# Kernel optimization log

Measured on AMD Instinct MI355X. Metric: run time of the kernel, lower is better.

## Reference

```python
import jax, jax.numpy as jnp
import numpy as np

B, N_LEAVES, HID, NCLS, VOCAB = 32, 512, 128, 2, 50257
N_NODES = 2 * N_LEAVES - 1  # complete binary tree, heap layout


def setup_inputs() -> dict:
    key = jax.random.key(0)
    ks = jax.random.split(key, 12)
    x = jax.random.randint(ks[0], (B, N_NODES), 0, VOCAB)
    cue = jax.random.randint(ks[1], (B, N_NODES), 0, NCLS)
    # word j sits at tree leaf node L-1+j
    word_index = jnp.tile(jnp.arange(N_LEAVES - 1, 2 * N_LEAVES - 1), (B, 1))
    # parent->child adjacency stored in adj[:, 1]
    A = np.zeros((2, N_NODES, N_NODES), dtype=bool)
    p = np.arange(N_LEAVES - 1)
    A[1, p, 2 * p + 1] = True
    A[1, p, 2 * p + 2] = True
    adj = jnp.asarray(np.broadcast_to(A, (B, 2, N_NODES, N_NODES)).copy())
    s = 0.05
    emb = jax.random.normal(ks[2], (VOCAB, HID - NCLS)) * s
    Wc = jax.random.normal(ks[3], (HID, 2 * HID)) * s
    bc = jax.random.normal(ks[4], (HID,)) * s
    Wd = jax.random.normal(ks[5], (2 * HID, 2 * HID)) * s
    bd = jax.random.normal(ks[6], (2 * HID,)) * s
    Wg = jax.random.normal(ks[7], (HID, HID)) * s
    bg = jax.random.normal(ks[8], (HID,)) * s
    Wcl = jax.random.normal(ks[9], (NCLS, 2 * HID)) * s
    bcl = jax.random.normal(ks[10], (NCLS,)) * s
    return dict(x=x, word_index=word_index, cue=cue, adj=adj, emb=emb,
                Wc=Wc, bc=bc, Wd=Wd, bd=bd, Wg=Wg, bg=bg, Wcl=Wcl, bcl=bcl)


def reference(x, word_index, cue, adj, emb, Wc, bc, Wd, bd, Wg, bg, Wcl, bcl):
    # adj encodes the same complete binary heap tree that is hardcoded below
    Bn, N = x.shape
    H = Wc.shape[0]
    C = bcl.shape[0]
    L = (N + 1) // 2
    depth = L.bit_length() - 1  # leaves live at level `depth`
    bidx = jnp.arange(Bn)[:, None]

    word_emb = emb[x]                                   # (B, N, H-C)
    cue_oh = jax.nn.one_hot(cue, C, dtype=word_emb.dtype)
    in_feats = jnp.concatenate([word_emb, cue_oh], -1)  # (B, N, H)
    sent = in_feats[bidx, word_index]                   # (B, L, H) leaf feats

    # ---- upward compose: level-batched bottom-up traversal ----
    h = jnp.zeros((Bn, N, H), in_feats.dtype).at[bidx, word_index].set(sent)
    for d in range(depth - 1, -1, -1):
        p = jnp.arange(2 ** d - 1, 2 ** (d + 1) - 1)
        ctx = jnp.concatenate([h[:, 2 * p + 1], h[:, 2 * p + 2]], -1)  # (B, 2^d, 2H)
        h = h.at[:, p].set(jnp.tanh(ctx @ Wc.T + bc))
    # upward_results never writes leaf rows -> leaves stay zero
    up = h.at[bidx, word_index].set(0.0)

    g_down = jax.nn.sigmoid(h[:, 0] @ Wg.T + bg)        # (B, H)

    # ---- downward decompose: level-batched top-down traversal ----
    down = jnp.zeros_like(h).at[:, 0].set(g_down)
    for d in range(depth):
        p = jnp.arange(2 ** d - 1, 2 ** (d + 1) - 1)
        ctx = jnp.concatenate([down[:, p], up[:, p]], -1)
        ch = jnp.tanh(ctx @ Wd.T + bd)                  # (B, 2^d, 2H)
        down = down.at[:, 2 * p + 1].set(ch[..., :H]).at[:, 2 * p + 2].set(ch[..., H:])

    tree = jnp.concatenate([down, up], -1)              # (B, N, 2H)
    scores = jax.nn.sigmoid(tree @ Wcl.T + bcl)
    return jax.nn.softmax(scores, -1)
```

## Files before the change

### kernel.cpp

```cpp
#include <hip/hip_runtime.h>
#include <hip/hip_fp16.h>


constexpr int NNODES = 1023;

typedef _Float16 h2 __attribute__((ext_vector_type(2)));

__device__ __forceinline__ float dot2(uint a, uint b, float c) {
  union { uint u; h2 h; } x, y;
  x.u = a; y.u = b;
  return __builtin_amdgcn_fdot2(x.h, y.h, c, false);
}

__device__ __forceinline__ uint f2h2(float a, float b) {
  return (uint)__half_as_ushort(__float2half_rn(a)) |
         ((uint)__half_as_ushort(__float2half_rn(b)) << 16);
}

__device__ __forceinline__ float2 h2f2(uint u) {
  union { uint u; h2 h; } c; c.u = u;
  return make_float2((float)c.h.x, (float)c.h.y);
}

__device__ __forceinline__ void load_wslice(const float* __restrict__ Wrow,
                                            int l16, int m, uint* wout) {
  const float4 f0 = *(const float4*)(Wrow + l16 * 8 + m * 128);
  const float4 f1 = *(const float4*)(Wrow + l16 * 8 + m * 128 + 4);
  wout[0] = f2h2(f0.x, f0.y);
  wout[1] = f2h2(f0.z, f0.w);
  wout[2] = f2h2(f1.x, f1.y);
  wout[3] = f2h2(f1.z, f1.w);
}

__device__ __forceinline__ float fold16(const float* a, int l) {
  float b[8];
#pragma unroll
  for (int u = 0; u < 8; ++u) {
    const float mine = (l & 1) ? a[2 * u + 1] : a[2 * u];
    const float oth  = (l & 1) ? a[2 * u]     : a[2 * u + 1];
    b[u] = mine + __shfl_xor(oth, 1);
  }
  float c[4];
#pragma unroll
  for (int u = 0; u < 4; ++u) {
    const float mine = (l & 2) ? b[2 * u + 1] : b[2 * u];
    const float oth  = (l & 2) ? b[2 * u]     : b[2 * u + 1];
    c[u] = mine + __shfl_xor(oth, 2);
  }
  float d[2];
#pragma unroll
  for (int u = 0; u < 2; ++u) {
    const float mine = (l & 4) ? c[2 * u + 1] : c[2 * u];
    const float oth  = (l & 4) ? c[2 * u]     : c[2 * u + 1];
    d[u] = mine + __shfl_xor(oth, 4);
  }
  const float mine = (l & 8) ? d[1] : d[0];
  const float oth  = (l & 8) ? d[0] : d[1];
  return mine + __shfl_xor(oth, 8);
}

__device__ __forceinline__ float fold8(const float* a, int l) {
  float b[4];
#pragma unroll
  for (int u = 0; u < 4; ++u) {
    const float mine = (l & 1) ? a[2 * u + 1] : a[2 * u];
    const float oth  = (l & 1) ? a[2 * u]     : a[2 * u + 1];
    b[u] = mine + __shfl_xor(oth, 1);
  }
  float c[2];
#pragma unroll
  for (int u = 0; u < 2; ++u) {
    const float mine = (l & 2) ? b[2 * u + 1] : b[2 * u];
    const float oth  = (l & 2) ? b[2 * u]     : b[2 * u + 1];
    c[u] = mine + __shfl_xor(oth, 2);
  }
  const float mine = (l & 4) ? c[1] : c[0];
  const float oth  = (l & 4) ? c[0] : c[1];
  return mine + __shfl_xor(oth, 4);
}

__device__ __forceinline__ float fold4(const float* a, int l) {
  float b[2];
#pragma unroll
  for (int u = 0; u < 2; ++u) {
    const float mine = (l & 1) ? a[2 * u + 1] : a[2 * u];
    const float oth  = (l & 1) ? a[2 * u]     : a[2 * u + 1];
    b[u] = mine + __shfl_xor(oth, 1);
  }
  const float mine = (l & 2) ? b[1] : b[0];
  const float oth  = (l & 2) ? b[0] : b[1];
  return mine + __shfl_xor(oth, 2);
}

template<int CH>
__device__ __forceinline__ float foldCH(const float (&a)[CH * 4], int l16) {
  if constexpr (CH == 4) {
    return fold16(a, l16);
  } else if constexpr (CH == 2) {
    float t = fold8(a, l16);
    t += __shfl_xor(t, 8);
    return t;
  } else {
    float t = fold4(a, l16);
    t += __shfl_xor(t, 4);
    t += __shfl_xor(t, 8);
    return t;
  }
}

template<int CH>
__device__ __forceinline__ void up_pass(uint* __restrict__ heap2, int base, int cb,
                                        int cbase, const uint (&w)[4][8],
                                        float bias_r, int g, int l16, bool wr) {
  float a[CH * 4];
#pragma unroll
  for (int v = 0; v < CH * 4; ++v) a[v] = 0.f;
#pragma unroll
  for (int p = 0; p < CH; ++p) {
    const uint* cp = heap2 + (cb + 2 * (cbase + p)) * 64 + l16 * 4;
#pragma unroll
    for (int m = 0; m < 2; ++m) {
      const uint4 cc = *(const uint4*)(cp + m * 64);
#pragma unroll
      for (int r = 0; r < 4; ++r) {
        float av = a[p * 4 + r];
        av = dot2(w[r][m * 4 + 0], cc.x, av);
        av = dot2(w[r][m * 4 + 1], cc.y, av);
        av = dot2(w[r][m * 4 + 2], cc.z, av);
        av = dot2(w[r][m * 4 + 3], cc.w, av);
        a[p * 4 + r] = av;
      }
    }
  }
  const float tot = foldCH<CH>(a, l16);
  if (wr && l16 < CH * 4) {
    _Float16* hH = (_Float16*)heap2;
    hH[(base + cbase + (l16 >> 2)) * 128 + 4 * g + (l16 & 3)] =
        (_Float16)tanhf(tot + bias_r);
  }
}

template<int NP, int NH>
__device__ __forceinline__ void up_level16(uint* __restrict__ heap2,
                                           const uint (&w)[4][8],
                                           float bias_r, int g, int l16, int ph) {
  constexpr int base = NP - 1, cb = 2 * NP - 1;
  if constexpr (NP >= 4 * NH) {
#pragma unroll
    for (int c0 = 0; c0 < NP; c0 += 4 * NH)
      up_pass<4>(heap2, base, cb, c0 + ph * 4, w, bias_r, g, l16, true);
  } else if constexpr (NP * 2 == 4 * NH) {
    up_pass<2>(heap2, base, cb, ph * 2, w, bias_r, g, l16, true);
  } else if constexpr (NP == NH) {
    up_pass<1>(heap2, base, cb, ph, w, bias_r, g, l16, true);
  } else {
    up_pass<1>(heap2, base, cb, 0, w, bias_r, g, l16, ph == 0);
  }
  __syncthreads();
}

template<int CH>
__device__ __forceinline__ void down_pass(uint* __restrict__ db2,
                                          const uint* __restrict__ ub2,
                                          int base, int cb, int cbase,
                                          const uint (&w)[4][8],
                                          float bias_r, int g, int l16) {
  float a[CH * 4];
#pragma unroll
  for (int v = 0; v < CH * 4; ++v) a[v] = 0.f;
#pragma unroll
  for (int p = 0; p < CH; ++p) {
    const uint* dp = db2 + (base + cbase + p) * 64 + l16 * 4;
    const uint* up = ub2 + (base + cbase + p) * 64 + l16 * 4;
    const uint4 c0 = *(const uint4*)dp;
    const uint4 c1 = *(const uint4*)up;
#pragma unroll
    for (int r = 0; r < 4; ++r) {
      float av = a[p * 4 + r];
      av = dot2(w[r][0], c0.x, av);
      av = dot2(w[r][1], c0.y, av);
      av = dot2(w[r][2], c0.z, av);
      av = dot2(w[r][3], c0.w, av);
      av = dot2(w[r][4], c1.x, av);
      av = dot2(w[r][5], c1.y, av);
      av = dot2(w[r][6], c1.z, av);
      av = dot2(w[r][7], c1.w, av);
      a[p * 4 + r] = av;
    }
  }
  const float tot = foldCH<CH>(a, l16);
  if (l16 < CH * 4) {
    const int row = 4 * g + (l16 & 3);
    ((_Float16*)db2)[(cb + 2 * (cbase + (l16 >> 2)) + (row >> 7)) * 128 + (row & 127)] =
        (_Float16)tanhf(tot + bias_r);
  }
}

template<int NP>
__device__ __forceinline__ void down_level16(uint* __restrict__ db2,
                                             const uint* __restrict__ ub2,
                                             const uint (&w)[4][8],
                                             float bias_r, int g, int l16) {
  constexpr int base = NP - 1, cb = 2 * NP - 1;
  if constexpr (NP >= 4) {
#pragma unroll
    for (int c0 = 0; c0 < NP; c0 += 4)
      down_pass<4>(db2, ub2, base, cb, c0, w, bias_r, g, l16);
  } else {
    down_pass<NP>(db2, ub2, base, cb, 0, w, bias_r, g, l16);
  }
  __syncthreads();
}

template<int NP>
__device__ __forceinline__ void down_level16_dual(uint* __restrict__ A0,
                                                  const uint* __restrict__ B0,
                                                  uint* __restrict__ A1,
                                                  const uint* __restrict__ B1,
                                                  const uint (&w)[4][8],
                                                  float bias_r, int g, int l16) {
  constexpr int base = NP - 1, cb = 2 * NP - 1;
  if constexpr (NP >= 4) {
#pragma unroll
    for (int c0 = 0; c0 < NP; c0 += 4) {
      down_pass<4>(A0, B0, base, cb, c0, w, bias_r, g, l16);
      down_pass<4>(A1, B1, base, cb, c0, w, bias_r, g, l16);
    }
  } else {
    down_pass<NP>(A0, B0, base, cb, 0, w, bias_r, g, l16);
    down_pass<NP>(A1, B1, base, cb, 0, w, bias_r, g, l16);
  }
  __syncthreads();
}

__device__ __forceinline__ void classify16(const uint* __restrict__ dn2,
                                           const uint* __restrict__ un2,
                                           const float* __restrict__ wcl,
                                           const float* __restrict__ bcl,
                                           float* __restrict__ o, int l16) {
  const int k0 = l16 * 8;
  float s0 = 0.f, s1 = 0.f;
  {
    const uint4 du = *(const uint4*)(dn2 + l16 * 4);
    const float2 d0 = h2f2(du.x), d1 = h2f2(du.y), d2 = h2f2(du.z), d3 = h2f2(du.w);
    s0 += d0.x * wcl[k0]     + d0.y * wcl[k0 + 1] + d1.x * wcl[k0 + 2] + d1.y * wcl[k0 + 3]
        + d2.x * wcl[k0 + 4] + d2.y * wcl[k0 + 5] + d3.x * wcl[k0 + 6] + d3.y * wcl[k0 + 7];
    s1 += d0.x * wcl[256 + k0]     + d0.y * wcl[256 + k0 + 1]
        + d1.x * wcl[256 + k0 + 2] + d1.y * wcl[256 + k0 + 3]
        + d2.x * wcl[256 + k0 + 4] + d2.y * wcl[256 + k0 + 5]
        + d3.x * wcl[256 + k0 + 6] + d3.y * wcl[256 + k0 + 7];
  }
  if (un2) {
    const uint4 uu = *(const uint4*)(un2 + l16 * 4);
    const float2 u0 = h2f2(uu.x), u1 = h2f2(uu.y), u2 = h2f2(uu.z), u3 = h2f2(uu.w);
    s0 += u0.x * wcl[128 + k0]     + u0.y * wcl[128 + k0 + 1]
        + u1.x * wcl[128 + k0 + 2] + u1.y * wcl[128 + k0 + 3]
        + u2.x * wcl[128 + k0 + 4] + u2.y * wcl[128 + k0 + 5]
        + u3.x * wcl[128 + k0 + 6] + u3.y * wcl[128 + k0 + 7];
    s1 += u0.x * wcl[384 + k0]     + u0.y * wcl[384 + k0 + 1]
        + u1.x * wcl[384 + k0 + 2] + u1.y * wcl[384 + k0 + 3]
        + u2.x * wcl[384 + k0 + 4] + u2.y * wcl[384 + k0 + 5]
        + u3.x * wcl[384 + k0 + 6] + u3.y * wcl[384 + k0 + 7];
  }
#pragma unroll
  for (int m = 8; m >= 1; m >>= 1) {
    s0 += __shfl_xor(s0, m);
    s1 += __shfl_xor(s1, m);
  }
  if (l16 == 0) {
    s0 += bcl[0]; s1 += bcl[1];
    const float p0 = 1.f / (1.f + expf(-s0));
    const float p1 = 1.f / (1.f + expf(-s1));
    const float mx = fmaxf(p0, p1);
    const float e0 = expf(p0 - mx), e1 = expf(p1 - mx);
    const float inv = 1.f / (e0 + e1);
    o[0] = e0 * inv;
    o[1] = e1 * inv;
  }
}

__global__ __launch_bounds__(512, 4) void kA_up(const int* __restrict__ x,
                                                const int* __restrict__ cue,
                                                const float* __restrict__ emb,
                                                const float* __restrict__ Wc,
                                                const float* __restrict__ bc,
                                                uint* __restrict__ hw) {
  __shared__ __align__(16) uint heap2[63 * 64];
  __shared__ __align__(16) uint pad[10240];
  const int b = blockIdx.x >> 4, s = blockIdx.x & 15, r = 15 + s;
  const int t = threadIdx.x, g = t >> 4, l16 = t & 15;
  if (t == 0) ((volatile uint*)pad)[0] = 0u;

  uint w[4][8];
#pragma unroll
  for (int rr = 0; rr < 4; ++rr)
#pragma unroll
    for (int m = 0; m < 2; ++m)
      load_wslice(Wc + (4 * g + rr) * 256, l16, m, &w[rr][m * 4]);
  const float bias_r = bc[4 * g + (l16 & 3)];

  for (int idx = t; idx < 32 * 64; idx += 512) {
    const int j = idx >> 6, c = idx & 63, k0 = 2 * c;
    const int gq = ((r + 1) << 5) - 1 + j;
    const int xi = x[b * NNODES + gq], ci = cue[b * NNODES + gq];
    const float v0 = (k0 < 126) ? emb[(long long)xi * 126 + k0]
                                : ((ci == (k0 - 126)) ? 1.f : 0.f);
    const float v1 = (k0 + 1 < 126) ? emb[(long long)xi * 126 + k0 + 1]
                                    : ((ci == (k0 + 1 - 126)) ? 1.f : 0.f);
    heap2[(31 + j) * 64 + c] = f2h2(v0, v1);
  }
  __syncthreads();

  up_level16<16, 1>(heap2, w, bias_r, g, l16, 0);
  up_level16<8, 1>(heap2, w, bias_r, g, l16, 0);
  up_level16<4, 1>(heap2, w, bias_r, g, l16, 0);
  up_level16<2, 1>(heap2, w, bias_r, g, l16, 0);
  up_level16<1, 1>(heap2, w, bias_r, g, l16, 0);

  uint4* dst = (uint4*)(hw + (size_t)(b * 16 + s) * 31 * 64);
  const uint4* src = (const uint4*)heap2;
  for (int idx = t; idx < 31 * 16; idx += 512) dst[idx] = src[idx];
}

__global__ __launch_bounds__(1024, 4) void kC_all(const float* __restrict__ Wc,
                                                  const float* __restrict__ bc,
                                                  const float* __restrict__ Wg,
                                                  const float* __restrict__ bg,
                                                  const float* __restrict__ Wd,
                                                  const float* __restrict__ bd,
                                                  const float* __restrict__ Wcl,
                                                  const float* __restrict__ bcl,
                                                  const uint* __restrict__ hw,
                                                  float* __restrict__ out) {
  __shared__ __align__(16) uint A2[2 * 63 * 64];
  __shared__ __align__(16) uint B2[2 * 31 * 64];
  __shared__ __align__(16) uint rootdn2[128];
  __shared__ __align__(16) float wcl[512];
  __shared__ __align__(16) uint pad[8192];
  const int b = blockIdx.x >> 3, sp = blockIdx.x & 7;
  const int t = threadIdx.x, g = t >> 4, l16 = t & 15;
  if (t == 0) ((volatile uint*)pad)[0] = 0u;
  uint* A1 = A2 + 63 * 64;
  uint* B1 = B2 + 31 * 64;

  for (int idx = t; idx < 16 * 16; idx += 1024) {
    const int s = idx >> 4, q = idx & 15;
    *((uint4*)(B2 + (15 + s) * 64) + q) =
        *((const uint4*)(hw + (size_t)(b * 16 + s) * 31 * 64) + q);
  }
  if (t < 512) wcl[t] = Wcl[t];
  __syncthreads();

  {
    const int gu = g & 31, ph = t >> 9;
    uint wu[4][8];
#pragma unroll
    for (int rr = 0; rr < 4; ++rr)
#pragma unroll
      for (int m = 0; m < 2; ++m)
        load_wslice(Wc + (4 * gu + rr) * 256, l16, m, &wu[rr][m * 4]);
    const float bias_u = bc[4 * gu + (l16 & 3)];
    up_level16<8, 2>(B2, wu, bias_u, gu, l16, ph);
    up_level16<4, 2>(B2, wu, bias_u, gu, l16, ph);
    up_level16<2, 2>(B2, wu, bias_u, gu, l16, ph);
    up_level16<1, 2>(B2, wu, bias_u, gu, l16, ph);

    uint wg[4][4];
#pragma unroll
    for (int rr = 0; rr < 4; ++rr)
      load_wslice(Wg + (4 * gu + rr) * 128, l16, 0, &wg[rr][0]);
    float a[4];
#pragma unroll
    for (int v = 0; v < 4; ++v) a[v] = 0.f;
    {
      const uint4 cc = *(const uint4*)(B2 + l16 * 4);
#pragma unroll
      for (int rr = 0; rr < 4; ++rr) {
        float av = a[rr];
        av = dot2(wg[rr][0], cc.x, av);
        av = dot2(wg[rr][1], cc.y, av);
        av = dot2(wg[rr][2], cc.z, av);
        av = dot2(wg[rr][3], cc.w, av);
        a[rr] = av;
      }
    }
    float tot = fold4(a, l16);
    tot += __shfl_xor(tot, 4);
    tot += __shfl_xor(tot, 8);
    if (ph == 0 && l16 < 4) {
      const int row = 4 * gu + l16;
      ((_Float16*)A2)[row] = (_Float16)(1.f / (1.f + expf(-(tot + bg[row]))));
    }
    __syncthreads();
  }
  asm volatile("" ::: "memory");

  uint w[4][8];
#pragma unroll
  for (int rr = 0; rr < 4; ++rr)
#pragma unroll
    for (int m = 0; m < 2; ++m)
      load_wslice(Wd + (4 * g + rr) * 256, l16, m, &w[rr][m * 4]);
  const float bias_r = bd[4 * g + (l16 & 3)];

  down_level16<1>(A2, B2, w, bias_r, g, l16);
  down_level16<2>(A2, B2, w, bias_r, g, l16);
  down_level16<4>(A2, B2, w, bias_r, g, l16);
  down_level16<8>(A2, B2, w, bias_r, g, l16);

  if (sp == 0 && t < 15 * 16) {
    const int m = t >> 4;
    classify16(A2 + m * 64, B2 + m * 64, wcl, bcl,
               out + ((size_t)b * NNODES + m) * 2, l16);
  }
  if (t < 128) rootdn2[t] = A2[(15 + sp * 2 + (t >> 6)) * 64 + (t & 63)];
  __syncthreads();

  for (int idx = t; idx < 2 * 31 * 16; idx += 1024) {
    const int ss = (idx >= 31 * 16) ? 1 : 0;
    const int k4 = idx - ss * 31 * 16;
    ((uint4*)(B2 + ss * 31 * 64))[k4] =
        ((const uint4*)(hw + (size_t)(b * 16 + sp * 2 + ss) * 31 * 64))[k4];
  }
  if (t < 128) A2[(t >> 6) * 63 * 64 + (t & 63)] = rootdn2[t];
  __syncthreads();

  down_level16_dual<1>(A2, B2, A1, B1, w, bias_r, g, l16);
  down_level16_dual<2>(A2, B2, A1, B1, w, bias_r, g, l16);
  down_level16_dual<4>(A2, B2, A1, B1, w, bias_r, g, l16);
  down_level16_dual<8>(A2, B2, A1, B1, w, bias_r, g, l16);
  down_level16_dual<16>(A2, B2, A1, B1, w, bias_r, g, l16);

  if (t < 63 * 16) {
    const int m = t >> 4;
    const int lvl = 31 - __clz(m + 1);
    const int j = (m + 1) - (1 << lvl);
#pragma unroll
    for (int ss = 0; ss < 2; ++ss) {
      const int r = 15 + sp * 2 + ss;
      const int gq = ((r + 1) << lvl) - 1 + j;
      classify16(A2 + ss * 63 * 64 + m * 64,
                 (m < 31) ? (B2 + ss * 31 * 64 + m * 64) : nullptr, wcl, bcl,
                 out + ((size_t)b * NNODES + gq) * 2, l16);
    }
  }
}

extern "C" void kernel_launch(void* const* d_in, const int* in_sizes, int n_in,
                              void* d_out, int out_size, void* d_ws, size_t ws_size,
                              hipStream_t stream) {
  const int*   x   = (const int*)d_in[0];
  const int*   cue = (const int*)d_in[2];
  const float* emb = (const float*)d_in[4];
  const float* Wc  = (const float*)d_in[5];
  const float* bc  = (const float*)d_in[6];
  const float* Wd  = (const float*)d_in[7];
  const float* bd  = (const float*)d_in[8];
  const float* Wg  = (const float*)d_in[9];
  const float* bg  = (const float*)d_in[10];
  const float* Wcl = (const float*)d_in[11];
  const float* bcl = (const float*)d_in[12];
  float* out = (float*)d_out;

  uint* hw = (uint*)d_ws;

  hipLaunchKernelGGL(kA_up,  dim3(512), dim3(512), 0, stream, x, cue, emb, Wc, bc, hw);
  hipLaunchKernelGGL(kC_all, dim3(256), dim3(1024), 0, stream,
                     Wc, bc, Wg, bg, Wd, bd, Wcl, bcl, hw, out);
}
```

Measured before the change: 70.38 us.

## Split downward pass into one 512-thread block per subtree with paired row weights

The second kernel now runs 512 blocks of 512 threads, each owning a single 32-leaf subtree, where before it ran 256 blocks of 1024 threads that each handled two subtrees. Each thread keeps weights for both output halves (rows r and r+128) and computes both child outputs in one pass, which doubles the per-thread weight registers. The top-of-tree upward/downward work (levels above the subtrees) is now recomputed redundantly by 16 blocks per batch instead of 8. This trades more redundant top-level work and register pressure for more, smaller blocks and higher occupancy.

```diff
diff --git a/kernel.cpp b/kernel.cpp
--- a/kernel.cpp
+++ b/kernel.cpp
@@ -111,7 +111,7 @@
 template<int CH>
 __device__ __forceinline__ void up_pass(uint* __restrict__ heap2, int base, int cb,
                                         int cbase, const uint (&w)[4][8],
-                                        float bias_r, int g, int l16, bool wr) {
+                                        float bias_r, int g, int l16) {
   float a[CH * 4];
 #pragma unroll
   for (int v = 0; v < CH * 4; ++v) a[v] = 0.f;
@@ -133,102 +133,88 @@
     }
   }
   const float tot = foldCH<CH>(a, l16);
-  if (wr && l16 < CH * 4) {
-    _Float16* hH = (_Float16*)heap2;
-    hH[(base + cbase + (l16 >> 2)) * 128 + 4 * g + (l16 & 3)] =
+  if (l16 < CH * 4) {
+    ((_Float16*)heap2)[(base + cbase + (l16 >> 2)) * 128 + 4 * g + (l16 & 3)] =
         (_Float16)tanhf(tot + bias_r);
   }
 }
 
-template<int NP, int NH>
-__device__ __forceinline__ void up_level16(uint* __restrict__ heap2,
-                                           const uint (&w)[4][8],
-                                           float bias_r, int g, int l16, int ph) {
-  constexpr int base = NP - 1, cb = 2 * NP - 1;
-  if constexpr (NP >= 4 * NH) {
-#pragma unroll
-    for (int c0 = 0; c0 < NP; c0 += 4 * NH)
-      up_pass<4>(heap2, base, cb, c0 + ph * 4, w, bias_r, g, l16, true);
-  } else if constexpr (NP * 2 == 4 * NH) {
-    up_pass<2>(heap2, base, cb, ph * 2, w, bias_r, g, l16, true);
-  } else if constexpr (NP == NH) {
-    up_pass<1>(heap2, base, cb, ph, w, bias_r, g, l16, true);
-  } else {
-    up_pass<1>(heap2, base, cb, 0, w, bias_r, g, l16, ph == 0);
-  }
-  __syncthreads();
-}
-
-template<int CH>
-__device__ __forceinline__ void down_pass(uint* __restrict__ db2,
-                                          const uint* __restrict__ ub2,
-                                          int base, int cb, int cbase,
-                                          const uint (&w)[4][8],
-                                          float bias_r, int g, int l16) {
-  float a[CH * 4];
-#pragma unroll
-  for (int v = 0; v < CH * 4; ++v) a[v] = 0.f;
-#pragma unroll
-  for (int p = 0; p < CH; ++p) {
-    const uint* dp = db2 + (base + cbase + p) * 64 + l16 * 4;
-    const uint* up = ub2 + (base + cbase + p) * 64 + l16 * 4;
-    const uint4 c0 = *(const uint4*)dp;
-    const uint4 c1 = *(const uint4*)up;
-#pragma unroll
-    for (int r = 0; r < 4; ++r) {
-      float av = a[p * 4 + r];
-      av = dot2(w[r][0], c0.x, av);
-      av = dot2(w[r][1], c0.y, av);
-      av = dot2(w[r][2], c0.z, av);
-      av = dot2(w[r][3], c0.w, av);
-      av = dot2(w[r][4], c1.x, av);
-      av = dot2(w[r][5], c1.y, av);
-      av = dot2(w[r][6], c1.z, av);
-      av = dot2(w[r][7], c1.w, av);
-      a[p * 4 + r] = av;
-    }
-  }
-  const float tot = foldCH<CH>(a, l16);
-  if (l16 < CH * 4) {
-    const int row = 4 * g + (l16 & 3);
-    ((_Float16*)db2)[(cb + 2 * (cbase + (l16 >> 2)) + (row >> 7)) * 128 + (row & 127)] =
-        (_Float16)tanhf(tot + bias_r);
-  }
-}
-
 template<int NP>
-__device__ __forceinline__ void down_level16(uint* __restrict__ db2,
-                                             const uint* __restrict__ ub2,
-                                             const uint (&w)[4][8],
-                                             float bias_r, int g, int l16) {
+__device__ __forceinline__ void up_level512(uint* __restrict__ heap2,
+                                            const uint (&w)[4][8],
+                                            float bias_r, int g, int l16) {
   constexpr int base = NP - 1, cb = 2 * NP - 1;
   if constexpr (NP >= 4) {
 #pragma unroll
     for (int c0 = 0; c0 < NP; c0 += 4)
-      down_pass<4>(db2, ub2, base, cb, c0, w, bias_r, g, l16);
+      up_pass<4>(heap2, base, cb, c0, w, bias_r, g, l16);
   } else {
-    down_pass<NP>(db2, ub2, base, cb, 0, w, bias_r, g, l16);
-  }
-  __syncthreads();
+    up_pass<NP>(heap2, base, cb, 0, w, bias_r, g, l16);
+  }
+  __syncthreads();
+}
+
+template<int CH>
+__device__ __forceinline__ void down_pass8(uint* __restrict__ db2,
+                                           const uint* __restrict__ ub2,
+                                           int base, int cb, int cbase,
+                                           const uint (&w)[2][4][8],
+                                           float bias0, float bias1,
+                                           int g, int l16) {
+  float a0[CH * 4], a1[CH * 4];
+#pragma unroll
+  for (int v = 0; v < CH * 4; ++v) { a0[v] = 0.f; a1[v] = 0.f; }
+#pragma unroll
+  for (int p = 0; p < CH; ++p) {
+    const uint4 c0 = *(const uint4*)(db2 + (base + cbase + p) * 64 + l16 * 4);
+    const uint4 c1 = *(const uint4*)(ub2 + (base + cbase + p) * 64 + l16 * 4);
+#pragma unroll
+    for (int r = 0; r < 4; ++r) {
+      float av = a0[p * 4 + r];
+      av = dot2(w[0][r][0], c0.x, av);
+      av = dot2(w[0][r][1], c0.y, av);
+      av = dot2(w[0][r][2], c0.z, av);
+      av = dot2(w[0][r][3], c0.w, av);
+      av = dot2(w[0][r][4], c1.x, av);
+      av = dot2(w[0][r][5], c1.y, av);
+      av = dot2(w[0][r][6], c1.z, av);
+      av = dot2(w[0][r][7], c1.w, av);
+      a0[p * 4 + r] = av;
+      float bv = a1[p * 4 + r];
+      bv = dot2(w[1][r][0], c0.x, bv);
+      bv = dot2(w[1][r][1], c0.y, bv);
+      bv = dot2(w[1][r][2], c0.z, bv);
+      bv = dot2(w[1][r][3], c0.w, bv);
+      bv = dot2(w[1][r][4], c1.x, bv);
+      bv = dot2(w[1][r][5], c1.y, bv);
+      bv = dot2(w[1][r][6], c1.z, bv);
+      bv = dot2(w[1][r][7], c1.w, bv);
+      a1[p * 4 + r] = bv;
+    }
+  }
+  const float t0 = foldCH<CH>(a0, l16);
+  const float t1 = foldCH<CH>(a1, l16);
+  if (l16 < CH * 4) {
+    const int p = l16 >> 2, col = 4 * g + (l16 & 3);
+    _Float16* dH = (_Float16*)db2;
+    dH[(cb + 2 * (cbase + p)) * 128 + col]     = (_Float16)tanhf(t0 + bias0);
+    dH[(cb + 2 * (cbase + p) + 1) * 128 + col] = (_Float16)tanhf(t1 + bias1);
+  }
 }
 
 template<int NP>
-__device__ __forceinline__ void down_level16_dual(uint* __restrict__ A0,
-                                                  const uint* __restrict__ B0,
-                                                  uint* __restrict__ A1,
-                                                  const uint* __restrict__ B1,
-                                                  const uint (&w)[4][8],
-                                                  float bias_r, int g, int l16) {
+__device__ __forceinline__ void down_level8(uint* __restrict__ db2,
+                                            const uint* __restrict__ ub2,
+                                            const uint (&w)[2][4][8],
+                                            float bias0, float bias1,
+                                            int g, int l16) {
   constexpr int base = NP - 1, cb = 2 * NP - 1;
   if constexpr (NP >= 4) {
 #pragma unroll
-    for (int c0 = 0; c0 < NP; c0 += 4) {
-      down_pass<4>(A0, B0, base, cb, c0, w, bias_r, g, l16);
-      down_pass<4>(A1, B1, base, cb, c0, w, bias_r, g, l16);
-    }
+    for (int c0 = 0; c0 < NP; c0 += 4)
+      down_pass8<4>(db2, ub2, base, cb, c0, w, bias0, bias1, g, l16);
   } else {
-    down_pass<NP>(A0, B0, base, cb, 0, w, bias_r, g, l16);
-    down_pass<NP>(A1, B1, base, cb, 0, w, bias_r, g, l16);
+    down_pass8<NP>(db2, ub2, base, cb, 0, w, bias0, bias1, g, l16);
   }
   __syncthreads();
 }
@@ -311,18 +297,18 @@
   }
   __syncthreads();
 
-  up_level16<16, 1>(heap2, w, bias_r, g, l16, 0);
-  up_level16<8, 1>(heap2, w, bias_r, g, l16, 0);
-  up_level16<4, 1>(heap2, w, bias_r, g, l16, 0);
-  up_level16<2, 1>(heap2, w, bias_r, g, l16, 0);
-  up_level16<1, 1>(heap2, w, bias_r, g, l16, 0);
+  up_level512<16>(heap2, w, bias_r, g, l16);
+  up_level512<8>(heap2, w, bias_r, g, l16);
+  up_level512<4>(heap2, w, bias_r, g, l16);
+  up_level512<2>(heap2, w, bias_r, g, l16);
+  up_level512<1>(heap2, w, bias_r, g, l16);
 
   uint4* dst = (uint4*)(hw + (size_t)(b * 16 + s) * 31 * 64);
   const uint4* src = (const uint4*)heap2;
   for (int idx = t; idx < 31 * 16; idx += 512) dst[idx] = src[idx];
 }
 
-__global__ __launch_bounds__(1024, 4) void kC_all(const float* __restrict__ Wc,
+__global__ __launch_bounds__(512, 4) void kS_down(const float* __restrict__ Wc,
                                                   const float* __restrict__ bc,
                                                   const float* __restrict__ Wg,
                                                   const float* __restrict__ bg,
@@ -332,43 +318,40 @@
                                                   const float* __restrict__ bcl,
                                                   const uint* __restrict__ hw,
                                                   float* __restrict__ out) {
-  __shared__ __align__(16) uint A2[2 * 63 * 64];
-  __shared__ __align__(16) uint B2[2 * 31 * 64];
-  __shared__ __align__(16) uint rootdn2[128];
+  __shared__ __align__(16) uint A2[63 * 64];
+  __shared__ __align__(16) uint B2[31 * 64];
+  __shared__ __align__(16) uint rootdn2[64];
   __shared__ __align__(16) float wcl[512];
-  __shared__ __align__(16) uint pad[8192];
-  const int b = blockIdx.x >> 3, sp = blockIdx.x & 7;
+  __shared__ __align__(16) uint pad[8500];
+  const int b = blockIdx.x >> 4, s = blockIdx.x & 15;
   const int t = threadIdx.x, g = t >> 4, l16 = t & 15;
   if (t == 0) ((volatile uint*)pad)[0] = 0u;
-  uint* A1 = A2 + 63 * 64;
-  uint* B1 = B2 + 31 * 64;
-
-  for (int idx = t; idx < 16 * 16; idx += 1024) {
-    const int s = idx >> 4, q = idx & 15;
-    *((uint4*)(B2 + (15 + s) * 64) + q) =
-        *((const uint4*)(hw + (size_t)(b * 16 + s) * 31 * 64) + q);
+
+  for (int idx = t; idx < 16 * 16; idx += 512) {
+    const int s2 = idx >> 4, q = idx & 15;
+    *((uint4*)(B2 + (15 + s2) * 64) + q) =
+        *((const uint4*)(hw + (size_t)(b * 16 + s2) * 31 * 64) + q);
   }
   if (t < 512) wcl[t] = Wcl[t];
   __syncthreads();
 
   {
-    const int gu = g & 31, ph = t >> 9;
     uint wu[4][8];
 #pragma unroll
     for (int rr = 0; rr < 4; ++rr)
 #pragma unroll
       for (int m = 0; m < 2; ++m)
-        load_wslice(Wc + (4 * gu + rr) * 256, l16, m, &wu[rr][m * 4]);
-    const float bias_u = bc[4 * gu + (l16 & 3)];
-    up_level16<8, 2>(B2, wu, bias_u, gu, l16, ph);
-    up_level16<4, 2>(B2, wu, bias_u, gu, l16, ph);
-    up_level16<2, 2>(B2, wu, bias_u, gu, l16, ph);
-    up_level16<1, 2>(B2, wu, bias_u, gu, l16, ph);
+        load_wslice(Wc + (4 * g + rr) * 256, l16, m, &wu[rr][m * 4]);
+    const float bias_u = bc[4 * g + (l16 & 3)];
+    up_level512<8>(B2, wu, bias_u, g, l16);
+    up_level512<4>(B2, wu, bias_u, g, l16);
+    up_level512<2>(B2, wu, bias_u, g, l16);
+    up_level512<1>(B2, wu, bias_u, g, l16);
 
     uint wg[4][4];
 #pragma unroll
     for (int rr = 0; rr < 4; ++rr)
-      load_wslice(Wg + (4 * gu + rr) * 128, l16, 0, &wg[rr][0]);
+      load_wslice(Wg + (4 * g + rr) * 128, l16, 0, &wg[rr][0]);
     float a[4];
 #pragma unroll
     for (int v = 0; v < 4; ++v) a[v] = 0.f;
@@ -387,60 +370,58 @@
     float tot = fold4(a, l16);
     tot += __shfl_xor(tot, 4);
     tot += __shfl_xor(tot, 8);
-    if (ph == 0 && l16 < 4) {
-      const int row = 4 * gu + l16;
+    if (l16 < 4) {
+      const int row = 4 * g + l16;
       ((_Float16*)A2)[row] = (_Float16)(1.f / (1.f + expf(-(tot + bg[row]))));
     }
     __syncthreads();
   }
   asm volatile("" ::: "memory");
 
-  uint w[4][8];
-#pragma unroll
-  for (int rr = 0; rr < 4; ++rr)
-#pragma unroll
-    for (int m = 0; m < 2; ++m)
-      load_wslice(Wd + (4 * g + rr) * 256, l16, m, &w[rr][m * 4]);
-  const float bias_r = bd[4 * g + (l16 & 3)];
-
-  down_level16<1>(A2, B2, w, bias_r, g, l16);
-  down_level16<2>(A2, B2, w, bias_r, g, l16);
-  down_level16<4>(A2, B2, w, bias_r, g, l16);
-  down_level16<8>(A2, B2, w, bias_r, g, l16);
-
-  if (sp == 0 && t < 15 * 16) {
+  uint w[2][4][8];
+#pragma unroll
+  for (int h = 0; h < 2; ++h)
+#pragma unroll
+    for (int rr = 0; rr < 4; ++rr)
+#pragma unroll
+      for (int m = 0; m < 2; ++m)
+        load_wslice(Wd + (h * 128 + 4 * g + rr) * 256, l16, m, &w[h][rr][m * 4]);
+  const float bias0 = bd[4 * g + (l16 & 3)];
+  const float bias1 = bd[128 + 4 * g + (l16 & 3)];
+
+  down_level8<1>(A2, B2, w, bias0, bias1, g, l16);
+  down_level8<2>(A2, B2, w, bias0, bias1, g, l16);
+  down_level8<4>(A2, B2, w, bias0, bias1, g, l16);
+  down_level8<8>(A2, B2, w, bias0, bias1, g, l16);
+
+  if (s == 0 && t < 15 * 16) {
     const int m = t >> 4;
     classify16(A2 + m * 64, B2 + m * 64, wcl, bcl,
                out + ((size_t)b * NNODES + m) * 2, l16);
   }
-  if (t < 128) rootdn2[t] = A2[(15 + sp * 2 + (t >> 6)) * 64 + (t & 63)];
-  __syncthreads();
-
-  for (int idx = t; idx < 2 * 31 * 16; idx += 1024) {
-    const int ss = (idx >= 31 * 16) ? 1 : 0;
-    const int k4 = idx - ss * 31 * 16;
-    ((uint4*)(B2 + ss * 31 * 64))[k4] =
-        ((const uint4*)(hw + (size_t)(b * 16 + sp * 2 + ss) * 31 * 64))[k4];
-  }
-  if (t < 128) A2[(t >> 6) * 63 * 64 + (t & 63)] = rootdn2[t];
-  __syncthreads();
-
-  down_level16_dual<1>(A2, B2, A1, B1, w, bias_r, g, l16);
-  down_level16_dual<2>(A2, B2, A1, B1, w, bias_r, g, l16);
-  down_level16_dual<4>(A2, B2, A1, B1, w, bias_r, g, l16);
-  down_level16_dual<8>(A2, B2, A1, B1, w, bias_r, g, l16);
-  down_level16_dual<16>(A2, B2, A1, B1, w, bias_r, g, l16);
-
-  if (t < 63 * 16) {
-    const int m = t >> 4;
-    const int lvl = 31 - __clz(m + 1);
-    const int j = (m + 1) - (1 << lvl);
-#pragma unroll
-    for (int ss = 0; ss < 2; ++ss) {
-      const int r = 15 + sp * 2 + ss;
+  if (t < 64) rootdn2[t] = A2[(15 + s) * 64 + t];
+  __syncthreads();
+
+  for (int idx = t; idx < 31 * 16; idx += 512)
+    ((uint4*)B2)[idx] = ((const uint4*)(hw + (size_t)(b * 16 + s) * 31 * 64))[idx];
+  if (t < 64) A2[t] = rootdn2[t];
+  __syncthreads();
+
+  down_level8<1>(A2, B2, w, bias0, bias1, g, l16);
+  down_level8<2>(A2, B2, w, bias0, bias1, g, l16);
+  down_level8<4>(A2, B2, w, bias0, bias1, g, l16);
+  down_level8<8>(A2, B2, w, bias0, bias1, g, l16);
+  down_level8<16>(A2, B2, w, bias0, bias1, g, l16);
+
+  const int r = 15 + s;
+#pragma unroll
+  for (int pass = 0; pass < 2; ++pass) {
+    const int m = (t >> 4) + pass * 32;
+    if (m < 63) {
+      const int lvl = 31 - __clz(m + 1);
+      const int j = (m + 1) - (1 << lvl);
       const int gq = ((r + 1) << lvl) - 1 + j;
-      classify16(A2 + ss * 63 * 64 + m * 64,
-                 (m < 31) ? (B2 + ss * 31 * 64 + m * 64) : nullptr, wcl, bcl,
+      classify16(A2 + m * 64, (m < 31) ? (B2 + m * 64) : nullptr, wcl, bcl,
                  out + ((size_t)b * NNODES + gq) * 2, l16);
     }
   }
@@ -464,7 +445,7 @@
 
   uint* hw = (uint*)d_ws;
 
-  hipLaunchKernelGGL(kA_up,  dim3(512), dim3(512), 0, stream, x, cue, emb, Wc, bc, hw);
-  hipLaunchKernelGGL(kC_all, dim3(256), dim3(1024), 0, stream,
+  hipLaunchKernelGGL(kA_up,   dim3(512), dim3(512), 0, stream, x, cue, emb, Wc, bc, hw);
+  hipLaunchKernelGGL(kS_down, dim3(512), dim3(512), 0, stream,
                      Wc, bc, Wg, bg, Wd, bd, Wcl, bcl, hw, out);
 }
```

Result: slower. 76.40 us (+8.6%).

## Fuse up and down passes into one cooperative kernel with grid syncs

Applied to the files above, without the earlier changes.

Replaces the two-kernel pipeline with a single cooperative kernel. Each 1024-thread block handles two subtrees, then exchanges subtree roots through global memory with grid-wide syncs instead of a second launch. Block 0 of each batch builds the top of the tree and the root-down state, and the leaf-level down pass now computes both child halves per thread group. This removes a launch and the round trip of full subtree heaps, at the cost of two grid barriers, idle blocks during the top-tree phase, and higher register use. The old two-kernel path is kept as a fallback if the cooperative launch fails.

```diff
diff --git a/kernel.cpp b/kernel.cpp
--- a/kernel.cpp
+++ b/kernel.cpp
@@ -1,5 +1,8 @@
 #include <hip/hip_runtime.h>
 #include <hip/hip_fp16.h>
+#include <hip/hip_cooperative_groups.h>
+
+namespace cg = cooperative_groups;
 
 
 constexpr int NNODES = 1023;
@@ -20,6 +23,13 @@
 __device__ __forceinline__ float2 h2f2(uint u) {
   union { uint u; h2 h; } c; c.u = u;
   return make_float2((float)c.h.x, (float)c.h.y);
+}
+
+__device__ __forceinline__ void gstore(uint* p, uint v) {
+  __hip_atomic_store(p, v, __ATOMIC_RELEASE, __HIP_MEMORY_SCOPE_AGENT);
+}
+__device__ __forceinline__ uint gload(const uint* p) {
+  return __hip_atomic_load(p, __ATOMIC_ACQUIRE, __HIP_MEMORY_SCOPE_AGENT);
 }
 
 __device__ __forceinline__ void load_wslice(const float* __restrict__ Wrow,
@@ -134,24 +144,38 @@
   }
   const float tot = foldCH<CH>(a, l16);
   if (wr && l16 < CH * 4) {
-    _Float16* hH = (_Float16*)heap2;
-    hH[(base + cbase + (l16 >> 2)) * 128 + 4 * g + (l16 & 3)] =
+    ((_Float16*)heap2)[(base + cbase + (l16 >> 2)) * 128 + 4 * g + (l16 & 3)] =
         (_Float16)tanhf(tot + bias_r);
   }
 }
 
-template<int NP, int NH>
-__device__ __forceinline__ void up_level16(uint* __restrict__ heap2,
-                                           const uint (&w)[4][8],
-                                           float bias_r, int g, int l16, int ph) {
+template<int NP>
+__device__ __forceinline__ void up_level512(uint* __restrict__ heap2,
+                                            const uint (&w)[4][8],
+                                            float bias_r, int g, int l16) {
   constexpr int base = NP - 1, cb = 2 * NP - 1;
-  if constexpr (NP >= 4 * NH) {
-#pragma unroll
-    for (int c0 = 0; c0 < NP; c0 += 4 * NH)
+  if constexpr (NP >= 4) {
+#pragma unroll
+    for (int c0 = 0; c0 < NP; c0 += 4)
+      up_pass<4>(heap2, base, cb, c0, w, bias_r, g, l16, true);
+  } else {
+    up_pass<NP>(heap2, base, cb, 0, w, bias_r, g, l16, true);
+  }
+  __syncthreads();
+}
+
+template<int NP>
+__device__ __forceinline__ void up_level16x2(uint* __restrict__ heap2,
+                                             const uint (&w)[4][8],
+                                             float bias_r, int g, int l16, int ph) {
+  constexpr int base = NP - 1, cb = 2 * NP - 1;
+  if constexpr (NP >= 8) {
+#pragma unroll
+    for (int c0 = 0; c0 < NP; c0 += 8)
       up_pass<4>(heap2, base, cb, c0 + ph * 4, w, bias_r, g, l16, true);
-  } else if constexpr (NP * 2 == 4 * NH) {
+  } else if constexpr (NP == 4) {
     up_pass<2>(heap2, base, cb, ph * 2, w, bias_r, g, l16, true);
-  } else if constexpr (NP == NH) {
+  } else if constexpr (NP == 2) {
     up_pass<1>(heap2, base, cb, ph, w, bias_r, g, l16, true);
   } else {
     up_pass<1>(heap2, base, cb, 0, w, bias_r, g, l16, ph == 0);
@@ -170,10 +194,8 @@
   for (int v = 0; v < CH * 4; ++v) a[v] = 0.f;
 #pragma unroll
   for (int p = 0; p < CH; ++p) {
-    const uint* dp = db2 + (base + cbase + p) * 64 + l16 * 4;
-    const uint* up = ub2 + (base + cbase + p) * 64 + l16 * 4;
-    const uint4 c0 = *(const uint4*)dp;
-    const uint4 c1 = *(const uint4*)up;
+    const uint4 c0 = *(const uint4*)(db2 + (base + cbase + p) * 64 + l16 * 4);
+    const uint4 c1 = *(const uint4*)(ub2 + (base + cbase + p) * 64 + l16 * 4);
 #pragma unroll
     for (int r = 0; r < 4; ++r) {
       float av = a[p * 4 + r];
@@ -229,6 +251,73 @@
   } else {
     down_pass<NP>(A0, B0, base, cb, 0, w, bias_r, g, l16);
     down_pass<NP>(A1, B1, base, cb, 0, w, bias_r, g, l16);
+  }
+  __syncthreads();
+}
+
+template<int CH>
+__device__ __forceinline__ void down_pass8(uint* __restrict__ db2,
+                                           const uint* __restrict__ ub2,
+                                           uint* __restrict__ wr,
+                                           int base, int cb, int cbase,
+                                           const uint (&w)[2][4][8],
+                                           float bias0, float bias1,
+                                           int g, int l16) {
+  float a0[CH * 4], a1[CH * 4];
+#pragma unroll
+  for (int v = 0; v < CH * 4; ++v) { a0[v] = 0.f; a1[v] = 0.f; }
+#pragma unroll
+  for (int p = 0; p < CH; ++p) {
+    const uint4 c0 = *(const uint4*)(db2 + (base + cbase + p) * 64 + l16 * 4);
+    const uint4 c1 = *(const uint4*)(ub2 + (base + cbase + p) * 64 + l16 * 4);
+#pragma unroll
+    for (int r = 0; r < 4; ++r) {
+      float av = a0[p * 4 + r];
+      av = dot2(w[0][r][0], c0.x, av);
+      av = dot2(w[0][r][1], c0.y, av);
+      av = dot2(w[0][r][2], c0.z, av);
+      av = dot2(w[0][r][3], c0.w, av);
+      av = dot2(w[0][r][4], c1.x, av);
+      av = dot2(w[0][r][5], c1.y, av);
+      av = dot2(w[0][r][6], c1.z, av);
+      av = dot2(w[0][r][7], c1.w, av);
+      a0[p * 4 + r] = av;
+      float bv = a1[p * 4 + r];
+      bv = dot2(w[1][r][0], c0.x, bv);
+      bv = dot2(w[1][r][1], c0.y, bv);
+      bv = dot2(w[1][r][2], c0.z, bv);
+      bv = dot2(w[1][r][3], c0.w, bv);
+      bv = dot2(w[1][r][4], c1.x, bv);
+      bv = dot2(w[1][r][5], c1.y, bv);
+      bv = dot2(w[1][r][6], c1.z, bv);
+      bv = dot2(w[1][r][7], c1.w, bv);
+      a1[p * 4 + r] = bv;
+    }
+  }
+  const float t0 = foldCH<CH>(a0, l16);
+  const float t1 = foldCH<CH>(a1, l16);
+  if (l16 < CH * 4) {
+    const int p = l16 >> 2, col = 4 * g + (l16 & 3);
+    _Float16* dH = (_Float16*)wr;
+    dH[(cb + 2 * (cbase + p)) * 128 + col]     = (_Float16)tanhf(t0 + bias0);
+    dH[(cb + 2 * (cbase + p) + 1) * 128 + col] = (_Float16)tanhf(t1 + bias1);
+  }
+}
+
+template<int NP>
+__device__ __forceinline__ void down_level8(uint* __restrict__ db2,
+                                            const uint* __restrict__ ub2,
+                                            uint* __restrict__ wr,
+                                            const uint (&w)[2][4][8],
+                                            float bias0, float bias1,
+                                            int g, int l16) {
+  constexpr int base = NP - 1, cb = 2 * NP - 1;
+  if constexpr (NP >= 4) {
+#pragma unroll
+    for (int c0 = 0; c0 < NP; c0 += 4)
+      down_pass8<4>(db2, ub2, wr, base, cb, c0, w, bias0, bias1, g, l16);
+  } else {
+    down_pass8<NP>(db2, ub2, wr, base, cb, 0, w, bias0, bias1, g, l16);
   }
   __syncthreads();
 }
@@ -279,7 +368,178 @@
   }
 }
 
-__global__ __launch_bounds__(512, 4) void kA_up(const int* __restrict__ x,
+__device__ __forceinline__ void gather_leaves(uint* __restrict__ heapX,
+                                              const int* __restrict__ x,
+                                              const int* __restrict__ cue,
+                                              const float* __restrict__ emb,
+                                              int b, int r, int tt, int stride) {
+  for (int idx = tt; idx < 32 * 64; idx += stride) {
+    const int j = idx >> 6, c = idx & 63, k0 = 2 * c;
+    const int gq = ((r + 1) << 5) - 1 + j;
+    const int xi = x[b * NNODES + gq], ci = cue[b * NNODES + gq];
+    const float v0 = (k0 < 126) ? emb[(long long)xi * 126 + k0]
+                                : ((ci == (k0 - 126)) ? 1.f : 0.f);
+    const float v1 = (k0 + 1 < 126) ? emb[(long long)xi * 126 + k0 + 1]
+                                    : ((ci == (k0 + 1 - 126)) ? 1.f : 0.f);
+    heapX[(31 + j) * 64 + c] = f2h2(v0, v1);
+  }
+}
+
+__global__ __launch_bounds__(1024, 4) void kFused(const int* __restrict__ x,
+                                                  const int* __restrict__ cue,
+                                                  const float* __restrict__ emb,
+                                                  const float* __restrict__ Wc,
+                                                  const float* __restrict__ bc,
+                                                  const float* __restrict__ Wg,
+                                                  const float* __restrict__ bg,
+                                                  const float* __restrict__ Wd,
+                                                  const float* __restrict__ bd,
+                                                  const float* __restrict__ Wcl,
+                                                  const float* __restrict__ bcl,
+                                                  uint* __restrict__ roots,
+                                                  uint* __restrict__ rootdn,
+                                                  float* __restrict__ out) {
+  __shared__ __align__(16) uint heapA[63 * 64];
+  __shared__ __align__(16) uint heapB[63 * 64];
+  __shared__ __align__(16) uint dbA[31 * 64];
+  __shared__ __align__(16) uint dbB[31 * 64];
+  __shared__ __align__(16) float wcl[512];
+  __shared__ __align__(16) uint pad[8448];
+  const int b = blockIdx.x >> 3, sp = blockIdx.x & 7;
+  const int t = threadIdx.x;
+  const int h = t >> 9, tt = t & 511, g = tt >> 4, l16 = t & 15;
+  const int s = sp * 2 + h, r = 15 + s;
+  uint* heapX = h ? heapB : heapA;
+  uint* dbX   = h ? dbB : dbA;
+  if (t == 0) ((volatile uint*)pad)[0] = 0u;
+  cg::grid_group grid = cg::this_grid();
+
+  uint wu[4][8];
+#pragma unroll
+  for (int rr = 0; rr < 4; ++rr)
+#pragma unroll
+    for (int m = 0; m < 2; ++m)
+      load_wslice(Wc + (4 * g + rr) * 256, l16, m, &wu[rr][m * 4]);
+  const float bias_u = bc[4 * g + (l16 & 3)];
+  if (t < 512) wcl[t] = Wcl[t];
+
+  gather_leaves(heapX, x, cue, emb, b, r, tt, 512);
+  __syncthreads();
+
+  up_level512<16>(heapX, wu, bias_u, g, l16);
+  up_level512<8>(heapX, wu, bias_u, g, l16);
+  up_level512<4>(heapX, wu, bias_u, g, l16);
+  up_level512<2>(heapX, wu, bias_u, g, l16);
+  up_level512<1>(heapX, wu, bias_u, g, l16);
+
+  if (tt < 64) gstore(&roots[(size_t)(b * 16 + s) * 64 + tt], heapX[tt]);
+  grid.sync();
+
+  if (sp == 0) {
+    uint* mub = dbA;
+    uint* mdb = dbB;
+    for (int idx = t; idx < 16 * 64; idx += 1024) {
+      const int s2 = idx >> 6, c = idx & 63;
+      mub[(15 + s2) * 64 + c] = gload(&roots[(size_t)(b * 16 + s2) * 64 + c]);
+    }
+    __syncthreads();
+
+    up_level16x2<8>(mub, wu, bias_u, g, l16, h);
+    up_level16x2<4>(mub, wu, bias_u, g, l16, h);
+    up_level16x2<2>(mub, wu, bias_u, g, l16, h);
+    up_level16x2<1>(mub, wu, bias_u, g, l16, h);
+
+    {
+      uint wg[4][4];
+#pragma unroll
+      for (int rr = 0; rr < 4; ++rr)
+        load_wslice(Wg + (4 * g + rr) * 128, l16, 0, &wg[rr][0]);
+      float a[4];
+#pragma unroll
+      for (int v = 0; v < 4; ++v) a[v] = 0.f;
+      const uint4 cc = *(const uint4*)(mub + l16 * 4);
+#pragma unroll
+      for (int rr = 0; rr < 4; ++rr) {
+        float av = a[rr];
+        av = dot2(wg[rr][0], cc.x, av);
+        av = dot2(wg[rr][1], cc.y, av);
+        av = dot2(wg[rr][2], cc.z, av);
+        av = dot2(wg[rr][3], cc.w, av);
+        a[rr] = av;
+      }
+      float tot = fold4(a, l16);
+      tot += __shfl_xor(tot, 4);
+      tot += __shfl_xor(tot, 8);
+      if (h == 0 && l16 < 4) {
+        const int row = 4 * g + l16;
+        ((_Float16*)mdb)[row] = (_Float16)(1.f / (1.f + expf(-(tot + bg[row]))));
+      }
+      __syncthreads();
+    }
+
+    {
+      const int gd = t >> 4;
+      uint wm[4][8];
+#pragma unroll
+      for (int rr = 0; rr < 4; ++rr)
+#pragma unroll
+        for (int m = 0; m < 2; ++m)
+          load_wslice(Wd + (4 * gd + rr) * 256, l16, m, &wm[rr][m * 4]);
+      const float bm = bd[4 * gd + (l16 & 3)];
+      down_level16<1>(mdb, mub, wm, bm, gd, l16);
+      down_level16<2>(mdb, mub, wm, bm, gd, l16);
+      down_level16<4>(mdb, mub, wm, bm, gd, l16);
+      down_level16<8>(mdb, mub, wm, bm, gd, l16);
+    }
+
+    if (t < 15 * 16) {
+      const int m = t >> 4;
+      classify16(mdb + m * 64, mub + m * 64, wcl, bcl,
+                 out + ((size_t)b * NNODES + m) * 2, l16);
+    }
+    for (int idx = t; idx < 16 * 64; idx += 1024) {
+      const int s2 = idx >> 6, c = idx & 63;
+      gstore(&rootdn[(size_t)(b * 16 + s2) * 64 + c], mdb[(15 + s2) * 64 + c]);
+    }
+  }
+  grid.sync();
+
+  asm volatile("" ::: "memory");
+  uint w8[2][4][8];
+#pragma unroll
+  for (int h2 = 0; h2 < 2; ++h2)
+#pragma unroll
+    for (int rr = 0; rr < 4; ++rr)
+#pragma unroll
+      for (int m = 0; m < 2; ++m)
+        load_wslice(Wd + (h2 * 128 + 4 * g + rr) * 256, l16, m, &w8[h2][rr][m * 4]);
+  const float bias0 = bd[4 * g + (l16 & 3)];
+  const float bias1 = bd[128 + 4 * g + (l16 & 3)];
+
+  if (tt < 64) dbX[tt] = gload(&rootdn[(size_t)(b * 16 + s) * 64 + tt]);
+  __syncthreads();
+
+  down_level8<1>(dbX, heapX, dbX, w8, bias0, bias1, g, l16);
+  down_level8<2>(dbX, heapX, dbX, w8, bias0, bias1, g, l16);
+  down_level8<4>(dbX, heapX, dbX, w8, bias0, bias1, g, l16);
+  down_level8<8>(dbX, heapX, dbX, w8, bias0, bias1, g, l16);
+  down_level8<16>(dbX, heapX, heapX, w8, bias0, bias1, g, l16);
+
+#pragma unroll
+  for (int pass = 0; pass < 2; ++pass) {
+    const int m = g + 32 * pass;
+    if (m < 63) {
+      const int lvl = 31 - __clz(m + 1);
+      const int j = (m + 1) - (1 << lvl);
+      const int gq = ((r + 1) << lvl) - 1 + j;
+      const uint* dn = (m < 31) ? (dbX + m * 64) : (heapX + m * 64);
+      const uint* un = (m < 31) ? (heapX + m * 64) : nullptr;
+      classify16(dn, un, wcl, bcl, out + ((size_t)b * NNODES + gq) * 2, l16);
+    }
+  }
+}
+
+__global__ __launch_bounds__(512, 4) void kA_fb(const int* __restrict__ x,
                                                 const int* __restrict__ cue,
                                                 const float* __restrict__ emb,
                                                 const float* __restrict__ Wc,
@@ -299,39 +559,30 @@
       load_wslice(Wc + (4 * g + rr) * 256, l16, m, &w[rr][m * 4]);
   const float bias_r = bc[4 * g + (l16 & 3)];
 
-  for (int idx = t; idx < 32 * 64; idx += 512) {
-    const int j = idx >> 6, c = idx & 63, k0 = 2 * c;
-    const int gq = ((r + 1) << 5) - 1 + j;
-    const int xi = x[b * NNODES + gq], ci = cue[b * NNODES + gq];
-    const float v0 = (k0 < 126) ? emb[(long long)xi * 126 + k0]
-                                : ((ci == (k0 - 126)) ? 1.f : 0.f);
-    const float v1 = (k0 + 1 < 126) ? emb[(long long)xi * 126 + k0 + 1]
-                                    : ((ci == (k0 + 1 - 126)) ? 1.f : 0.f);
-    heap2[(31 + j) * 64 + c] = f2h2(v0, v1);
-  }
-  __syncthreads();
-
-  up_level16<16, 1>(heap2, w, bias_r, g, l16, 0);
-  up_level16<8, 1>(heap2, w, bias_r, g, l16, 0);
-  up_level16<4, 1>(heap2, w, bias_r, g, l16, 0);
-  up_level16<2, 1>(heap2, w, bias_r, g, l16, 0);
-  up_level16<1, 1>(heap2, w, bias_r, g, l16, 0);
+  gather_leaves(heap2, x, cue, emb, b, r, t, 512);
+  __syncthreads();
+
+  up_level512<16>(heap2, w, bias_r, g, l16);
+  up_level512<8>(heap2, w, bias_r, g, l16);
+  up_level512<4>(heap2, w, bias_r, g, l16);
+  up_level512<2>(heap2, w, bias_r, g, l16);
+  up_level512<1>(heap2, w, bias_r, g, l16);
 
   uint4* dst = (uint4*)(hw + (size_t)(b * 16 + s) * 31 * 64);
   const uint4* src = (const uint4*)heap2;
   for (int idx = t; idx < 31 * 16; idx += 512) dst[idx] = src[idx];
 }
 
-__global__ __launch_bounds__(1024, 4) void kC_all(const float* __restrict__ Wc,
-                                                  const float* __restrict__ bc,
-                                                  const float* __restrict__ Wg,
-                                                  const float* __restrict__ bg,
-                                                  const float* __restrict__ Wd,
-                                                  const float* __restrict__ bd,
-                                                  const float* __restrict__ Wcl,
-                                                  const float* __restrict__ bcl,
-                                                  const uint* __restrict__ hw,
-                                                  float* __restrict__ out) {
+__global__ __launch_bounds__(1024, 4) void kC_fb(const float* __restrict__ Wc,
+                                                 const float* __restrict__ bc,
+                                                 const float* __restrict__ Wg,
+                                                 const float* __restrict__ bg,
+                                                 const float* __restrict__ Wd,
+                                                 const float* __restrict__ bd,
+                                                 const float* __restrict__ Wcl,
+                                                 const float* __restrict__ bcl,
+                                                 const uint* __restrict__ hw,
+                                                 float* __restrict__ out) {
   __shared__ __align__(16) uint A2[2 * 63 * 64];
   __shared__ __align__(16) uint B2[2 * 31 * 64];
   __shared__ __align__(16) uint rootdn2[128];
@@ -360,10 +611,10 @@
       for (int m = 0; m < 2; ++m)
         load_wslice(Wc + (4 * gu + rr) * 256, l16, m, &wu[rr][m * 4]);
     const float bias_u = bc[4 * gu + (l16 & 3)];
-    up_level16<8, 2>(B2, wu, bias_u, gu, l16, ph);
-    up_level16<4, 2>(B2, wu, bias_u, gu, l16, ph);
-    up_level16<2, 2>(B2, wu, bias_u, gu, l16, ph);
-    up_level16<1, 2>(B2, wu, bias_u, gu, l16, ph);
+    up_level16x2<8>(B2, wu, bias_u, gu, l16, ph);
+    up_level16x2<4>(B2, wu, bias_u, gu, l16, ph);
+    up_level16x2<2>(B2, wu, bias_u, gu, l16, ph);
+    up_level16x2<1>(B2, wu, bias_u, gu, l16, ph);
 
     uint wg[4][4];
 #pragma unroll
@@ -372,17 +623,15 @@
     float a[4];
 #pragma unroll
     for (int v = 0; v < 4; ++v) a[v] = 0.f;
-    {
-      const uint4 cc = *(const uint4*)(B2 + l16 * 4);
-#pragma unroll
-      for (int rr = 0; rr < 4; ++rr) {
-        float av = a[rr];
-        av = dot2(wg[rr][0], cc.x, av);
-        av = dot2(wg[rr][1], cc.y, av);
-        av = dot2(wg[rr][2], cc.z, av);
-        av = dot2(wg[rr][3], cc.w, av);
-        a[rr] = av;
-      }
+    const uint4 cc = *(const uint4*)(B2 + l16 * 4);
+#pragma unroll
+    for (int rr = 0; rr < 4; ++rr) {
+      float av = a[rr];
+      av = dot2(wg[rr][0], cc.x, av);
+      av = dot2(wg[rr][1], cc.y, av);
+      av = dot2(wg[rr][2], cc.z, av);
+      av = dot2(wg[rr][3], cc.w, av);
+      a[rr] = av;
     }
     float tot = fold4(a, l16);
     tot += __shfl_xor(tot, 4);
@@ -462,9 +711,20 @@
   const float* bcl = (const float*)d_in[12];
   float* out = (float*)d_out;
 
-  uint* hw = (uint*)d_ws;
-
-  hipLaunchKernelGGL(kA_up,  dim3(512), dim3(512), 0, stream, x, cue, emb, Wc, bc, hw);
-  hipLaunchKernelGGL(kC_all, dim3(256), dim3(1024), 0, stream,
-                     Wc, bc, Wg, bg, Wd, bd, Wcl, bcl, hw, out);
-}
+  uint* roots  = (uint*)d_ws;
+  uint* rootdn = roots + 32 * 16 * 64;
+  uint* hw     = rootdn + 32 * 16 * 64;
+
+  void* args[] = {(void*)&x, (void*)&cue, (void*)&emb, (void*)&Wc, (void*)&bc,
+                  (void*)&Wg, (void*)&bg, (void*)&Wd, (void*)&bd,
+                  (void*)&Wcl, (void*)&bcl, (void*)&roots, (void*)&rootdn,
+                  (void*)&out};
+  hipError_t e = hipLaunchCooperativeKernel((const void*)kFused, dim3(256),
+                                            dim3(1024), args, 0, stream);
+  if (e != hipSuccess) {
+    hipLaunchKernelGGL(kA_fb, dim3(512), dim3(512), 0, stream,
+                       x, cue, emb, Wc, bc, hw);
+    hipLaunchKernelGGL(kC_fb, dim3(256), dim3(1024), 0, stream,
+                       Wc, bc, Wg, bg, Wd, bd, Wcl, bcl, hw, out);
+  }
+}
```

Result: slower. 204.7 us (+190.9%).
